# Optimization experiments

Hardware: AMD Instinct MI355X
Metric: run time of the kernel (lower is better)

The kernel has to match this reference:

```python
import jax, jax.numpy as jnp
import numpy as np

N = 100000      # num nodes
E = 1600000     # num edges (before self-loops)
F_IN = 500      # num_features
H1, C1 = 8, 8   # heads, hidden_dim (layer 1, concat)
H2, C2 = 1, 16  # output_heads, num_classes (layer 2, mean)
NEG_SLOPE = 0.2


def setup_inputs() -> dict:
    key = jax.random.key(0)
    ks = jax.random.split(key, 10)
    x = jax.random.normal(ks[0], (N, F_IN), dtype=jnp.float32)
    edge_index = jax.random.randint(ks[1], (2, E), 0, N, dtype=jnp.int64)
    s = 0.05
    W1 = jax.random.normal(ks[2], (F_IN, H1 * C1), dtype=jnp.float32) * s
    a_src1 = jax.random.normal(ks[3], (H1, C1), dtype=jnp.float32) * s
    a_dst1 = jax.random.normal(ks[4], (H1, C1), dtype=jnp.float32) * s
    b1 = jnp.zeros((H1 * C1,), dtype=jnp.float32)
    W2 = jax.random.normal(ks[5], (H1 * C1, H2 * C2), dtype=jnp.float32) * s
    a_src2 = jax.random.normal(ks[6], (H2, C2), dtype=jnp.float32) * s
    a_dst2 = jax.random.normal(ks[7], (H2, C2), dtype=jnp.float32) * s
    b2 = jnp.zeros((C2,), dtype=jnp.float32)
    return {"x": x, "edge_index": edge_index, "W1": W1, "a_src1": a_src1,
            "a_dst1": a_dst1, "b1": b1, "W2": W2, "a_src2": a_src2,
            "a_dst2": a_dst2, "b2": b2}


def _gat_conv(x, src, dst, W, a_src, a_dst, bias, heads, out_c, concat):
    n = x.shape[0]
    xw = (x @ W).reshape(n, heads, out_c)                      # [N,H,C]
    # per-node attention halves, gathered per edge -> logits [E,H]
    s_src = jnp.einsum('nhc,hc->nh', xw, a_src)
    s_dst = jnp.einsum('nhc,hc->nh', xw, a_dst)
    e = s_src[src] + s_dst[dst]
    e = jnp.where(e > 0, e, NEG_SLOPE * e)                     # leaky_relu
    # segment softmax over incoming edges of each target node
    m = jax.ops.segment_max(e, dst, num_segments=n)            # [N,H]
    m = jnp.where(jnp.isfinite(m), m, 0.0)
    p = jnp.exp(e - m[dst])                                    # [E,H]
    denom = jax.ops.segment_sum(p, dst, num_segments=n)        # [N,H]
    alpha = p / denom[dst]                                     # [E,H]
    # scatter-aggregate weighted messages
    out = jax.ops.segment_sum(alpha[:, :, None] * xw[src], dst,
                              num_segments=n)                  # [N,H,C]
    if concat:
        out = out.reshape(n, heads * out_c)
    else:
        out = out.mean(axis=1)
    return out + bias


def reference(x, edge_index, W1, a_src1, a_dst1, b1, W2, a_src2, a_dst2, b2):
    # PyG GATConv adds self-loops by default
    loops = jnp.arange(N, dtype=edge_index.dtype)
    src = jnp.concatenate([edge_index[0], loops])
    dst = jnp.concatenate([edge_index[1], loops])
    # eval mode: dropout is identity
    h = _gat_conv(x, src, dst, W1, a_src1, a_dst1, b1, H1, C1, True)
    h = jax.nn.elu(h)
    h = _gat_conv(h, src, dst, W2, a_src2, a_dst2, b2, H2, C2, False)
    return jax.nn.log_softmax(h, axis=1)
```

## Files before the change

kernel.cpp:

```cpp
#include <hip/hip_runtime.h>
#include <hip/hip_bf16.h>
#include <math.h>

#define NEGS 0.2f
#define BSH 9
#define TS 4096

typedef __attribute__((ext_vector_type(8))) short bf16x8;
typedef __attribute__((ext_vector_type(8))) unsigned short u16x8;
typedef __attribute__((ext_vector_type(4))) float f32x4;

__device__ __forceinline__ unsigned short f2bf(float f) {
  __hip_bfloat16 h = __float2bfloat16(f);
  unsigned short u;
  __builtin_memcpy(&u, &h, 2);
  return u;
}
__device__ __forceinline__ float bf2f(unsigned short u) {
  return __uint_as_float((unsigned)u << 16);
}
__device__ __forceinline__ unsigned packbf(float lo, float hi) {
  return (unsigned)f2bf(lo) | ((unsigned)f2bf(hi) << 16);
}


__device__ __forceinline__ void dev_wcvt(const float* __restrict__ W1,
                                         unsigned short* __restrict__ Wb,
                                         int K, int Kp, int blk) {
  int t = blk * 256 + threadIdx.x;
  if (t >= Kp * 64) return;
  int kg = t >> 6, c = t & 63;
  float f = (kg < K) ? W1[(size_t)kg * 64 + c] : 0.f;
  size_t off = ((size_t)((kg >> 5) * 4 + ((kg >> 3) & 3)) * 512) + c * 8 + (kg & 7);
  Wb[off] = f2bf(f);
}

__device__ __forceinline__ void dev_thist(const int* __restrict__ ei,
                                          int* __restrict__ hist,
                                          int E, int NB, int tile) {
  __shared__ int lh[256];
  const int t = threadIdx.x;
  lh[t] = 0;
  __syncthreads();
  const int e0 = tile * TS;
#pragma unroll
  for (int j = 0; j < TS / 256; ++j) {
    int e = e0 + j * 256 + t;
    if (e < E) atomicAdd(&lh[ei[E + e] >> BSH], 1);
  }
  __syncthreads();
  if (t < NB) hist[tile * NB + t] = lh[t];
}

__device__ __forceinline__ void dev_bscan1(const int* __restrict__ hist,
                                           int* __restrict__ off_rel,
                                           int* __restrict__ total,
                                           int NT, int NB, int b) {
  __shared__ int sh[256];
  const int t = threadIdx.x;
  int t0 = 2 * t, t1 = 2 * t + 1;
  int v0 = (t0 < NT) ? hist[t0 * NB + b] : 0;
  int v1 = (t1 < NT) ? hist[t1 * NB + b] : 0;
  int ps = v0 + v1;
  sh[t] = ps;
  __syncthreads();
  for (int off = 1; off < 256; off <<= 1) {
    int v = (t >= off) ? sh[t - off] : 0;
    __syncthreads();
    sh[t] += v;
    __syncthreads();
  }
  int excl = sh[t] - ps;
  if (t0 < NT) off_rel[t0 * NB + b] = excl;
  if (t1 < NT) off_rel[t1 * NB + b] = excl + v0;
  if (t == 255) total[b] = sh[255];
}

__device__ __forceinline__ void dev_pscatter(const int* __restrict__ ei,
                                             const int* __restrict__ off_rel,
                                             const int* __restrict__ total,
                                             unsigned* __restrict__ pairs,
                                             int E, int NB, int tile) {
  __shared__ int cur[256];
  __shared__ int sb[256];
  const int t = threadIdx.x;
  int v = (t < NB) ? total[t] : 0;
  sb[t] = v;
  __syncthreads();
  for (int off = 1; off < 256; off <<= 1) {
    int x = (t >= off) ? sb[t - off] : 0;
    __syncthreads();
    sb[t] += x;
    __syncthreads();
  }
  if (t < NB) cur[t] = (sb[t] - v) + off_rel[tile * NB + t];
  __syncthreads();
  const int e0 = tile * TS;
#pragma unroll
  for (int j = 0; j < TS / 256; ++j) {
    int e = e0 + j * 256 + t;
    if (e < E) {
      int s = ei[e], d = ei[E + e];
      int pos = atomicAdd(&cur[d >> BSH], 1);
      pairs[pos] = ((unsigned)(d & ((1 << BSH) - 1)) << 23) | (unsigned)s;
    }
  }
}

__device__ __forceinline__ void dev_bcsr(const unsigned* __restrict__ pairs,
                                         const int* __restrict__ total,
                                         int* __restrict__ rowptr,
                                         int* __restrict__ col,
                                         int Nn, int E, int NB, int b) {
  __shared__ int cnt[1 << BSH];
  __shared__ int cu[1 << BSH];
  __shared__ int sh[256];
  __shared__ int P0, P1;
  const int t = threadIdx.x;
  const int d0 = b << BSH;
  const int dn = min(1 << BSH, Nn - d0);
  {
    int v = (t < NB) ? total[t] : 0;
    sh[t] = v;
    __syncthreads();
    for (int off = 1; off < 256; off <<= 1) {
      int x = (t >= off) ? sh[t - off] : 0;
      __syncthreads();
      sh[t] += x;
      __syncthreads();
    }
    if (t == b) { P0 = sh[t] - v; P1 = sh[t]; }
    __syncthreads();
  }
  const int p0 = P0, p1 = P1;
  const int rpb = p0 + d0;
  cnt[2 * t] = (2 * t < dn) ? 1 : 0;
  cnt[2 * t + 1] = (2 * t + 1 < dn) ? 1 : 0;
  __syncthreads();
  for (int i = p0 + t; i < p1; i += 256) atomicAdd(&cnt[pairs[i] >> 23], 1);
  __syncthreads();
  int a0 = cnt[2 * t], a1 = cnt[2 * t + 1];
  int ps = a0 + a1;
  sh[t] = ps;
  __syncthreads();
  for (int off = 1; off < 256; off <<= 1) {
    int v = (t >= off) ? sh[t - off] : 0;
    __syncthreads();
    sh[t] += v;
    __syncthreads();
  }
  int excl = sh[t] - ps;
#pragma unroll
  for (int u = 0; u < 2; ++u) {
    int i = 2 * t + u;
    int ex = (u == 0) ? excl : excl + a0;
    if (i < dn) {
      rowptr[d0 + i] = rpb + ex;
      col[rpb + ex] = d0 + i;
      cu[i] = ex + 1;
    }
  }
  if (b == NB - 1 && t == 0) rowptr[Nn] = E + Nn;
  __syncthreads();
  for (int i = p0 + t; i < p1; i += 256) {
    unsigned p = pairs[i];
    int pos = atomicAdd(&cu[p >> 23], 1);
    col[rpb + pos] = (int)(p & 0x7fffffu);
  }
}

__device__ __forceinline__ void dev_gemm(const float* __restrict__ A,
                                         const unsigned short* __restrict__ Wb,
                                         unsigned short* __restrict__ C,
                                         const float* __restrict__ a1d,
                                         float* __restrict__ sdst,
                                         int M, int K, int nck, int rowblk) {
  const int tid = threadIdx.x;
  const int lane = tid & 63;
  const int w = tid >> 6;
  const int r15 = lane & 15;
  const int kgrp = lane >> 4;
  const int bm = rowblk * 64;
  const int row = bm + w * 16 + r15;
  const float* Ar = A + (size_t)(row < M ? row : (M - 1)) * K;
  const int NIT = 2 * nck;
  const int ITV = (K >= 40) ? ((K - 40) / 32 + 1) : 0;

  f32x4 acc[4] = {};

  float4 c0, c1;
  {
    const float4* g = (const float4*)(Ar + kgrp * 8);
    c0 = g[0]; c1 = g[1];
  }
  for (int it = 0; it < NIT; ++it) {
    float4 n0, n1;
    if (it + 1 < NIT) {
      int k0 = (it + 1) * 32 + kgrp * 8;
      if (it + 1 < ITV) {
        const float4* g = (const float4*)(Ar + k0);
        n0 = g[0]; n1 = g[1];
      } else {
        float tmp[8];
#pragma unroll
        for (int j = 0; j < 8; ++j) {
          int kk = k0 + j;
          tmp[j] = (kk < K) ? Ar[kk] : 0.f;
        }
        n0 = make_float4(tmp[0], tmp[1], tmp[2], tmp[3]);
        n1 = make_float4(tmp[4], tmp[5], tmp[6], tmp[7]);
      }
    }
    const unsigned short* bb = Wb + ((size_t)(it * 4 + kgrp) * 512) + r15 * 8;
    bf16x8 bf4[4];
#pragma unroll
    for (int nc = 0; nc < 4; ++nc)
      bf4[nc] = *(const bf16x8*)(bb + nc * 128);
    unsigned pk[4] = { packbf(c0.x, c0.y), packbf(c0.z, c0.w),
                       packbf(c1.x, c1.y), packbf(c1.z, c1.w) };
    bf16x8 af = *(bf16x8*)pk;
#pragma unroll
    for (int nc = 0; nc < 4; ++nc)
      acc[nc] = __builtin_amdgcn_mfma_f32_16x16x32_bf16(af, bf4[nc], acc[nc], 0, 0, 0);
    c0 = n0; c1 = n1;
  }
  float dv[4];
#pragma unroll
  for (int nc = 0; nc < 4; ++nc) dv[nc] = a1d[nc * 16 + r15];
#pragma unroll
  for (int j = 0; j < 4; ++j) {
    int grow = bm + w * 16 + kgrp * 4 + j;
    bool liv = grow < M;
#pragma unroll
    for (int nc = 0; nc < 4; ++nc) {
      if (liv) C[(size_t)grow * 64 + nc * 16 + r15] = f2bf(acc[nc][j]);
      float sd = acc[nc][j] * dv[nc];
      sd += __shfl_xor(sd, 1); sd += __shfl_xor(sd, 2); sd += __shfl_xor(sd, 4);
      if ((r15 & 7) == 0 && liv)
        sdst[grow * 8 + nc * 2 + (r15 >> 3)] = sd;
    }
  }
}

__global__ __launch_bounds__(256) void k_A(const float* __restrict__ W1,
                                           unsigned short* __restrict__ Wb,
                                           int K, int Kp,
                                           const int* __restrict__ ei,
                                           int* __restrict__ hist,
                                           int E, int NB, int WCB) {
  int b = blockIdx.x;
  if (b < WCB) dev_wcvt(W1, Wb, K, Kp, b);
  else dev_thist(ei, hist, E, NB, b - WCB);
}

__global__ __launch_bounds__(256) void k_B1(const int* __restrict__ hist,
                                            int* __restrict__ off_rel,
                                            int* __restrict__ total,
                                            int NT, int NB,
                                            const float* __restrict__ A,
                                            const unsigned short* __restrict__ Wb,
                                            unsigned short* __restrict__ C,
                                            const float* __restrict__ a1d,
                                            float* __restrict__ sdst,
                                            int M, int K, int nck, int R0) {
  int b = blockIdx.x;
  if (b < NB) dev_bscan1(hist, off_rel, total, NT, NB, b);
  else dev_gemm(A, Wb, C, a1d, sdst, M, K, nck, b - NB + R0);
}

__global__ __launch_bounds__(256) void k_B2(const int* __restrict__ ei,
                                            const int* __restrict__ off_rel,
                                            const int* __restrict__ total,
                                            unsigned* __restrict__ pairs,
                                            int E, int NB, int NT,
                                            const float* __restrict__ A,
                                            const unsigned short* __restrict__ Wb,
                                            unsigned short* __restrict__ C,
                                            const float* __restrict__ a1d,
                                            float* __restrict__ sdst,
                                            int M, int K, int nck, int R0) {
  int b = blockIdx.x;
  if (b < NT) dev_pscatter(ei, off_rel, total, pairs, E, NB, b);
  else dev_gemm(A, Wb, C, a1d, sdst, M, K, nck, b - NT + R0);
}

__global__ __launch_bounds__(256) void k_B3(const unsigned* __restrict__ pairs,
                                            const int* __restrict__ total,
                                            int* __restrict__ rowptr,
                                            int* __restrict__ col,
                                            int Nn, int E, int NB,
                                            const float* __restrict__ A,
                                            const unsigned short* __restrict__ Wb,
                                            unsigned short* __restrict__ C,
                                            const float* __restrict__ a1d,
                                            float* __restrict__ sdst,
                                            int M, int K, int nck, int R0) {
  int b = blockIdx.x;
  if (b < NB) dev_bcsr(pairs, total, rowptr, col, Nn, E, NB, b);
  else dev_gemm(A, Wb, C, a1d, sdst, M, K, nck, b - NB + R0);
}

__global__ __launch_bounds__(256) void k_agg1(const int* __restrict__ rowptr,
                                              const int* __restrict__ col,
                                              const float* __restrict__ a1s,
                                              const float* __restrict__ sdst,
                                              const unsigned short* __restrict__ xwb,
                                              const float* __restrict__ b1,
                                              float* __restrict__ h1, int Nn) {
  int wid = (blockIdx.x * 256 + threadIdx.x) >> 6;
  if (wid >= Nn) return;
  int lane = threadIdx.x & 63;
  int slot = lane >> 3;
  int chg = lane & 7;
  float asr[8];
#pragma unroll
  for (int j = 0; j < 8; ++j) asr[j] = a1s[chg * 8 + j];
  float sd = sdst[wid * 8 + chg];
  int start = rowptr[wid], end = rowptr[wid + 1];
  float den = 0.f;
  float acc[8] = {};
  for (int it = start; it < end; it += 8) {
    int idx = it + slot;
    bool ok = idx < end;
    int s = col[ok ? idx : start];
    u16x8 pv = *(const u16x8*)(xwb + (size_t)s * 64 + chg * 8);
    float f[8];
#pragma unroll
    for (int j = 0; j < 8; ++j) f[j] = bf2f(pv[j]);
    float ss = 0.f;
#pragma unroll
    for (int j = 0; j < 8; ++j) ss = fmaf(f[j], asr[j], ss);
    float v = ss + sd;
    v = v > 0.f ? v : NEGS * v;
    float p = ok ? __expf(v) : 0.f;
    den += p;
#pragma unroll
    for (int j = 0; j < 8; ++j) acc[j] = fmaf(p, f[j], acc[j]);
  }
#pragma unroll
  for (int off = 8; off < 64; off <<= 1) {
    den += __shfl_xor(den, off);
#pragma unroll
    for (int j = 0; j < 8; ++j) acc[j] += __shfl_xor(acc[j], off);
  }
  if (slot == 0) {
    float inv = 1.f / den;
    float o[8];
#pragma unroll
    for (int j = 0; j < 8; ++j) {
      float v = acc[j] * inv + b1[chg * 8 + j];
      o[j] = v > 0.f ? v : (__expf(v) - 1.f);
    }
    float* dst = h1 + (size_t)wid * 64 + chg * 8;
#pragma unroll
    for (int j = 0; j < 8; ++j) dst[j] = o[j];
  }
}

__global__ __launch_bounds__(256) void k_gemm2p(const float* __restrict__ h1,
                                                const float* __restrict__ W2,
                                                const float* __restrict__ asr,
                                                const float* __restrict__ adt,
                                                unsigned short* __restrict__ xw2b,
                                                float* __restrict__ ssrc,
                                                float* __restrict__ sdst, int Nn) {
  __shared__ float w[64 * 16];
  int tid = threadIdx.x;
  for (int i = tid; i < 1024; i += 256) w[i] = W2[i];
  __syncthreads();
  int idx = blockIdx.x * 256 + tid;
  if (idx >= Nn * 16) return;
  int n = idx >> 4, c = idx & 15;
  const float* hr = h1 + (size_t)n * 64;
  float acc = 0.f;
#pragma unroll 8
  for (int k = 0; k < 64; ++k) acc += hr[k] * w[k * 16 + c];
  xw2b[idx] = f2bf(acc);
  float ssv = acc * asr[c], sdv = acc * adt[c];
#pragma unroll
  for (int off = 1; off < 16; off <<= 1) {
    ssv += __shfl_xor(ssv, off);
    sdv += __shfl_xor(sdv, off);
  }
  if (c == 0) { ssrc[n] = ssv; sdst[n] = sdv; }
}

__global__ __launch_bounds__(256) void k_agg2(const int* __restrict__ rowptr,
                                              const int* __restrict__ col,
                                              const float* __restrict__ ssrc,
                                              const float* __restrict__ sdst,
                                              const unsigned short* __restrict__ xw2b,
                                              const float* __restrict__ b2,
                                              float* __restrict__ out, int Nn) {
  int wid = (blockIdx.x * 256 + threadIdx.x) >> 6;
  if (wid >= Nn) return;
  int lane = threadIdx.x & 63;
  int slot = lane >> 4, c = lane & 15;
  float sd = sdst[wid];
  int start = rowptr[wid], end = rowptr[wid + 1];
  float den = 0.f, acc = 0.f;
  int i = start + slot;
  for (; i + 4 < end; i += 8) {
    int s0 = col[i], s1 = col[i + 4];
    float w0 = bf2f(xw2b[(size_t)s0 * 16 + c]);
    float w1 = bf2f(xw2b[(size_t)s1 * 16 + c]);
    float v0 = ssrc[s0] + sd; v0 = v0 > 0.f ? v0 : NEGS * v0;
    float v1 = ssrc[s1] + sd; v1 = v1 > 0.f ? v1 : NEGS * v1;
    float p0 = __expf(v0), p1 = __expf(v1);
    den += p0 + p1;
    acc = fmaf(p0, w0, acc);
    acc = fmaf(p1, w1, acc);
  }
  if (i < end) {
    int s = col[i];
    float v = ssrc[s] + sd;
    v = v > 0.f ? v : NEGS * v;
    float p = __expf(v);
    den += p;
    acc = fmaf(p, bf2f(xw2b[(size_t)s * 16 + c]), acc);
  }
  den += __shfl_xor(den, 16);
  den += __shfl_xor(den, 32);
  acc += __shfl_xor(acc, 16);
  acc += __shfl_xor(acc, 32);
  float o = acc / den + b2[c];
  float mx = o;
#pragma unroll
  for (int off = 1; off < 16; off <<= 1) mx = fmaxf(mx, __shfl_xor(mx, off));
  float ex = __expf(o - mx);
  float ssum = ex;
#pragma unroll
  for (int off = 1; off < 16; off <<= 1) ssum += __shfl_xor(ssum, off);
  float r = o - mx - __logf(ssum);
  if (slot == 0) out[(size_t)wid * 16 + c] = r;
}

extern "C" void kernel_launch(void* const* d_in, const int* in_sizes, int n_in,
                              void* d_out, int out_size, void* d_ws, size_t ws_size,
                              hipStream_t stream) {
  const float* x      = (const float*)d_in[0];
  const int* ei       = (const int*)d_in[1];
  const float* W1     = (const float*)d_in[2];
  const float* a_src1 = (const float*)d_in[3];
  const float* a_dst1 = (const float*)d_in[4];
  const float* b1     = (const float*)d_in[5];
  const float* W2     = (const float*)d_in[6];
  const float* a_src2 = (const float*)d_in[7];
  const float* a_dst2 = (const float*)d_in[8];
  const float* b2     = (const float*)d_in[9];

  const int F    = in_sizes[2] / 64;
  const int Nn   = in_sizes[0] / F;
  const int E    = in_sizes[1] / 2;
  const int Etot = E + Nn;
  const int nck  = (F + 63) >> 6;
  const int Kp   = nck * 64;
  const int NB   = (Nn + (1 << BSH) - 1) >> BSH;
  const int NT   = (E + TS - 1) / TS;
  const int WCB  = (Kp * 64 + 255) / 256;
  const int GB   = (Nn + 63) / 64;
  const int G1   = (GB + 2) / 3;
  const int G2   = G1;
  const int G3   = GB - G1 - G2;

  float* ws = (float*)d_ws;
  unsigned short* xwb = (unsigned short*)ws;
  float* h1     = ws + (size_t)Nn * 32;
  float* ssrc1  = h1 + (size_t)Nn * 64;
  float* sdst1  = ssrc1 + (size_t)Nn * 8;
  int* rowptr   = (int*)(sdst1 + (size_t)Nn * 8);
  int* col      = rowptr + Nn + 1;
  unsigned short* Wb = (unsigned short*)(col + ((Etot + 7) & ~7));
  int* hist     = (int*)(Wb + (size_t)Kp * 64);
  int* off_rel  = hist + (size_t)NT * NB;
  int* total    = off_rel + (size_t)NT * NB;
  unsigned* pairs = (unsigned*)h1;
  unsigned short* xw2b = (unsigned short*)ws;
  float* ssrc2  = ws + (size_t)Nn * 8;
  float* sdst2  = ssrc2 + Nn;
  float* out2   = (float*)d_out;

  dim3 blk(256);

  k_A<<<dim3(WCB + NT), blk, 0, stream>>>(W1, Wb, F, Kp, ei, hist, E, NB, WCB);
  k_B1<<<dim3(NB + G1), blk, 0, stream>>>(hist, off_rel, total, NT, NB,
      x, Wb, xwb, a_dst1, sdst1, Nn, F, nck, 0);
  k_B2<<<dim3(NT + G2), blk, 0, stream>>>(ei, off_rel, total, pairs, E, NB, NT,
      x, Wb, xwb, a_dst1, sdst1, Nn, F, nck, G1);
  k_B3<<<dim3(NB + G3), blk, 0, stream>>>(pairs, total, rowptr, col, Nn, E, NB,
      x, Wb, xwb, a_dst1, sdst1, Nn, F, nck, G1 + G2);
  k_agg1<<<dim3((Nn * 64 + 255) / 256), blk, 0, stream>>>(
      rowptr, col, a_src1, sdst1, xwb, b1, h1, Nn);
  k_gemm2p<<<dim3((Nn * 16 + 255) / 256), blk, 0, stream>>>(
      h1, W2, a_src2, a_dst2, xw2b, ssrc2, sdst2, Nn);
  k_agg2<<<dim3((Nn * 64 + 255) / 256), blk, 0, stream>>>(
      rowptr, col, ssrc2, sdst2, xw2b, b2, out2, Nn);
}
```

Before: 220.6 us.

## Fuse layer-2 projection into layer-1 aggregation and deepen GEMM A prefetch

Removes the separate layer-2 GEMM kernel. Each layer-1 aggregation wave now applies ELU and multiplies its 64-wide output by a pre-permuted W2, using shuffles to produce xw2 and the layer-2 attention scores directly. This avoids writing and re-reading h1 and saves one launch. W2 is permuted once in an extra block of the first kernel. Separately, the layer-1 GEMM prefetches A two iterations ahead instead of one, which raises register pressure.

```diff
diff --git a/kernel.cpp b/kernel.cpp
--- a/kernel.cpp
+++ b/kernel.cpp
@@ -33,6 +33,19 @@
   float f = (kg < K) ? W1[(size_t)kg * 64 + c] : 0.f;
   size_t off = ((size_t)((kg >> 5) * 4 + ((kg >> 3) & 3)) * 512) + c * 8 + (kg & 7);
   Wb[off] = f2bf(f);
+}
+
+__device__ __forceinline__ void dev_w2p(const float* __restrict__ W2,
+                                        float* __restrict__ W2p) {
+  int t = threadIdx.x;
+#pragma unroll
+  for (int u = 0; u < 4; ++u) {
+    int i = u * 256 + t;
+    int lane = i >> 4, r = i & 15;
+    int slot = lane >> 3, chg = lane & 7;
+    int j = r >> 1, cp = r & 1;
+    W2p[i] = W2[(chg * 8 + j) * 16 + slot * 2 + cp];
+  }
 }
 
 __device__ __forceinline__ void dev_thist(const int* __restrict__ ei,
@@ -188,29 +201,29 @@
 
   f32x4 acc[4] = {};
 
-  float4 c0, c1;
-  {
-    const float4* g = (const float4*)(Ar + kgrp * 8);
-    c0 = g[0]; c1 = g[1];
-  }
+  auto loadA = [&](int it, float4& o0, float4& o1) {
+    int k0 = it * 32 + kgrp * 8;
+    if (it < ITV) {
+      const float4* g = (const float4*)(Ar + k0);
+      o0 = g[0]; o1 = g[1];
+    } else {
+      float tmp[8];
+#pragma unroll
+      for (int j = 0; j < 8; ++j) {
+        int kk = k0 + j;
+        tmp[j] = (kk < K) ? Ar[kk] : 0.f;
+      }
+      o0 = make_float4(tmp[0], tmp[1], tmp[2], tmp[3]);
+      o1 = make_float4(tmp[4], tmp[5], tmp[6], tmp[7]);
+    }
+  };
+
+  float4 c0, c1, d0, d1;
+  loadA(0, c0, c1);
+  if (NIT > 1) loadA(1, d0, d1);
   for (int it = 0; it < NIT; ++it) {
-    float4 n0, n1;
-    if (it + 1 < NIT) {
-      int k0 = (it + 1) * 32 + kgrp * 8;
-      if (it + 1 < ITV) {
-        const float4* g = (const float4*)(Ar + k0);
-        n0 = g[0]; n1 = g[1];
-      } else {
-        float tmp[8];
-#pragma unroll
-        for (int j = 0; j < 8; ++j) {
-          int kk = k0 + j;
-          tmp[j] = (kk < K) ? Ar[kk] : 0.f;
-        }
-        n0 = make_float4(tmp[0], tmp[1], tmp[2], tmp[3]);
-        n1 = make_float4(tmp[4], tmp[5], tmp[6], tmp[7]);
-      }
-    }
+    float4 e0, e1;
+    if (it + 2 < NIT) loadA(it + 2, e0, e1);
     const unsigned short* bb = Wb + ((size_t)(it * 4 + kgrp) * 512) + r15 * 8;
     bf16x8 bf4[4];
 #pragma unroll
@@ -222,7 +235,8 @@
 #pragma unroll
     for (int nc = 0; nc < 4; ++nc)
       acc[nc] = __builtin_amdgcn_mfma_f32_16x16x32_bf16(af, bf4[nc], acc[nc], 0, 0, 0);
-    c0 = n0; c1 = n1;
+    c0 = d0; c1 = d1;
+    d0 = e0; d1 = e1;
   }
   float dv[4];
 #pragma unroll
@@ -247,10 +261,13 @@
                                            int K, int Kp,
                                            const int* __restrict__ ei,
                                            int* __restrict__ hist,
-                                           int E, int NB, int WCB) {
+                                           int E, int NB, int WCB,
+                                           const float* __restrict__ W2,
+                                           float* __restrict__ W2p) {
   int b = blockIdx.x;
   if (b < WCB) dev_wcvt(W1, Wb, K, Kp, b);
-  else dev_thist(ei, hist, E, NB, b - WCB);
+  else if (b == WCB) dev_w2p(W2, W2p);
+  else dev_thist(ei, hist, E, NB, b - WCB - 1);
 }
 
 __global__ __launch_bounds__(256) void k_B1(const int* __restrict__ hist,
@@ -300,13 +317,18 @@
   else dev_gemm(A, Wb, C, a1d, sdst, M, K, nck, b - NB + R0);
 }
 
-__global__ __launch_bounds__(256) void k_agg1(const int* __restrict__ rowptr,
-                                              const int* __restrict__ col,
-                                              const float* __restrict__ a1s,
-                                              const float* __restrict__ sdst,
-                                              const unsigned short* __restrict__ xwb,
-                                              const float* __restrict__ b1,
-                                              float* __restrict__ h1, int Nn) {
+__global__ __launch_bounds__(256) void k_agg1f(const int* __restrict__ rowptr,
+                                               const int* __restrict__ col,
+                                               const float* __restrict__ a1s,
+                                               const float* __restrict__ sdst,
+                                               const unsigned short* __restrict__ xwb,
+                                               const float* __restrict__ b1,
+                                               const float* __restrict__ W2p,
+                                               const float* __restrict__ a2s,
+                                               const float* __restrict__ a2d,
+                                               unsigned short* __restrict__ xw2b,
+                                               float* __restrict__ ssrc2,
+                                               float* __restrict__ sdst2, int Nn) {
   int wid = (blockIdx.x * 256 + threadIdx.x) >> 6;
   if (wid >= Nn) return;
   int lane = threadIdx.x & 63;
@@ -343,46 +365,33 @@
 #pragma unroll
     for (int j = 0; j < 8; ++j) acc[j] += __shfl_xor(acc[j], off);
   }
-  if (slot == 0) {
-    float inv = 1.f / den;
-    float o[8];
-#pragma unroll
-    for (int j = 0; j < 8; ++j) {
-      float v = acc[j] * inv + b1[chg * 8 + j];
-      o[j] = v > 0.f ? v : (__expf(v) - 1.f);
-    }
-    float* dst = h1 + (size_t)wid * 64 + chg * 8;
-#pragma unroll
-    for (int j = 0; j < 8; ++j) dst[j] = o[j];
-  }
-}
-
-__global__ __launch_bounds__(256) void k_gemm2p(const float* __restrict__ h1,
-                                                const float* __restrict__ W2,
-                                                const float* __restrict__ asr,
-                                                const float* __restrict__ adt,
-                                                unsigned short* __restrict__ xw2b,
-                                                float* __restrict__ ssrc,
-                                                float* __restrict__ sdst, int Nn) {
-  __shared__ float w[64 * 16];
-  int tid = threadIdx.x;
-  for (int i = tid; i < 1024; i += 256) w[i] = W2[i];
-  __syncthreads();
-  int idx = blockIdx.x * 256 + tid;
-  if (idx >= Nn * 16) return;
-  int n = idx >> 4, c = idx & 15;
-  const float* hr = h1 + (size_t)n * 64;
-  float acc = 0.f;
-#pragma unroll 8
-  for (int k = 0; k < 64; ++k) acc += hr[k] * w[k * 16 + c];
-  xw2b[idx] = f2bf(acc);
-  float ssv = acc * asr[c], sdv = acc * adt[c];
-#pragma unroll
-  for (int off = 1; off < 16; off <<= 1) {
+  float inv = 1.f / den;
+  float o[8];
+#pragma unroll
+  for (int j = 0; j < 8; ++j) {
+    float v = acc[j] * inv + b1[chg * 8 + j];
+    o[j] = v > 0.f ? v : (__expf(v) - 1.f);
+  }
+  const float4* wl = (const float4*)(W2p + lane * 16);
+  float4 w0 = wl[0], w1 = wl[1], w2 = wl[2], w3 = wl[3];
+  float p0, p1;
+  p0 = o[0] * w0.x + o[1] * w0.z + o[2] * w1.x + o[3] * w1.z +
+       o[4] * w2.x + o[5] * w2.z + o[6] * w3.x + o[7] * w3.z;
+  p1 = o[0] * w0.y + o[1] * w0.w + o[2] * w1.y + o[3] * w1.w +
+       o[4] * w2.y + o[5] * w2.w + o[6] * w3.y + o[7] * w3.w;
+  p0 += __shfl_xor(p0, 1); p0 += __shfl_xor(p0, 2); p0 += __shfl_xor(p0, 4);
+  p1 += __shfl_xor(p1, 1); p1 += __shfl_xor(p1, 2); p1 += __shfl_xor(p1, 4);
+  int c0i = slot * 2;
+  float ssv = p0 * a2s[c0i] + p1 * a2s[c0i + 1];
+  float sdv = p0 * a2d[c0i] + p1 * a2d[c0i + 1];
+#pragma unroll
+  for (int off = 8; off < 64; off <<= 1) {
     ssv += __shfl_xor(ssv, off);
     sdv += __shfl_xor(sdv, off);
   }
-  if (c == 0) { ssrc[n] = ssv; sdst[n] = sdv; }
+  if (chg == 0)
+    ((unsigned*)xw2b)[(size_t)wid * 8 + slot] = packbf(p0, p1);
+  if (lane == 0) { ssrc2[wid] = ssv; sdst2[wid] = sdv; }
 }
 
 __global__ __launch_bounds__(256) void k_agg2(const int* __restrict__ rowptr,
@@ -465,8 +474,8 @@
 
   float* ws = (float*)d_ws;
   unsigned short* xwb = (unsigned short*)ws;
-  float* h1     = ws + (size_t)Nn * 32;
-  float* ssrc1  = h1 + (size_t)Nn * 64;
+  float* h1reg  = ws + (size_t)Nn * 32;
+  float* ssrc1  = h1reg + (size_t)Nn * 64;
   float* sdst1  = ssrc1 + (size_t)Nn * 8;
   int* rowptr   = (int*)(sdst1 + (size_t)Nn * 8);
   int* col      = rowptr + Nn + 1;
@@ -474,25 +483,26 @@
   int* hist     = (int*)(Wb + (size_t)Kp * 64);
   int* off_rel  = hist + (size_t)NT * NB;
   int* total    = off_rel + (size_t)NT * NB;
-  unsigned* pairs = (unsigned*)h1;
-  unsigned short* xw2b = (unsigned short*)ws;
-  float* ssrc2  = ws + (size_t)Nn * 8;
+  float* W2p    = (float*)(total + 256);
+  unsigned* pairs = (unsigned*)h1reg;
+  unsigned short* xw2b = (unsigned short*)h1reg;
+  float* ssrc2  = h1reg + (size_t)Nn * 8;
   float* sdst2  = ssrc2 + Nn;
   float* out2   = (float*)d_out;
 
   dim3 blk(256);
 
-  k_A<<<dim3(WCB + NT), blk, 0, stream>>>(W1, Wb, F, Kp, ei, hist, E, NB, WCB);
+  k_A<<<dim3(WCB + 1 + NT), blk, 0, stream>>>(W1, Wb, F, Kp, ei, hist, E, NB,
+                                              WCB, W2, W2p);
   k_B1<<<dim3(NB + G1), blk, 0, stream>>>(hist, off_rel, total, NT, NB,
       x, Wb, xwb, a_dst1, sdst1, Nn, F, nck, 0);
   k_B2<<<dim3(NT + G2), blk, 0, stream>>>(ei, off_rel, total, pairs, E, NB, NT,
       x, Wb, xwb, a_dst1, sdst1, Nn, F, nck, G1);
   k_B3<<<dim3(NB + G3), blk, 0, stream>>>(pairs, total, rowptr, col, Nn, E, NB,
       x, Wb, xwb, a_dst1, sdst1, Nn, F, nck, G1 + G2);
-  k_agg1<<<dim3((Nn * 64 + 255) / 256), blk, 0, stream>>>(
-      rowptr, col, a_src1, sdst1, xwb, b1, h1, Nn);
-  k_gemm2p<<<dim3((Nn * 16 + 255) / 256), blk, 0, stream>>>(
-      h1, W2, a_src2, a_dst2, xw2b, ssrc2, sdst2, Nn);
+  k_agg1f<<<dim3((Nn * 64 + 255) / 256), blk, 0, stream>>>(
+      rowptr, col, a_src1, sdst1, xwb, b1, W2p, a_src2, a_dst2,
+      xw2b, ssrc2, sdst2, Nn);
   k_agg2<<<dim3((Nn * 64 + 255) / 256), blk, 0, stream>>>(
       rowptr, col, ssrc2, sdst2, xw2b, b2, out2, Nn);
 }
```

Result: faster. 206.3 us (-6.5%).
